# Kernel optimization log

Measured on AMD Instinct MI355X. Metric: run time of the kernel, lower is better.

The kernel has to match this reference:

```python
import jax, jax.numpy as jnp
import numpy as np

B, T, C, H = 2048, 128, 256, 64

def setup_inputs() -> dict:
    key = jax.random.key(0)
    kx, kk, kq, kv = jax.random.split(key, 4)
    s = 1.0 / np.sqrt(C)  # nn.Linear default init scale (approx)
    return {
        "x": jax.random.normal(kx, (B, T, C), dtype=jnp.float32),
        "Wk": jax.random.uniform(kk, (C, H), jnp.float32, -s, s),
        "Wq": jax.random.uniform(kq, (C, H), jnp.float32, -s, s),
        "Wv": jax.random.uniform(kv, (C, H), jnp.float32, -s, s),
    }

def reference(x, Wk, Wq, Wv):
    # x: [B,T,C]; projections to [B,T,H]
    k = jnp.einsum('btc,ch->bth', x, Wk)
    q = jnp.einsum('btc,ch->bth', x, Wq)
    v = jnp.einsum('btc,ch->bth', x, Wv)
    # NOTE: original scales by C**-0.5 (input dim), not head_size**-0.5
    scale = jnp.asarray(C, x.dtype) ** -0.5
    wei = jnp.einsum('bth,bsh->bts', q, k) * scale  # [B,T,T]
    causal = jnp.tril(jnp.ones((T, T), dtype=bool))
    wei = jnp.where(causal, wei, -jnp.inf)
    wei = jax.nn.softmax(wei, axis=-1)
    # dropout is identity in eval mode (deterministic reference)
    return jnp.einsum('bts,bsh->bth', wei, v)
```

## Files before the change

kernel.cpp:

```cpp
#include <hip/hip_runtime.h>

typedef __bf16 bf16;
typedef __bf16 bf16x4 __attribute__((ext_vector_type(4)));
typedef __bf16 bf16x8 __attribute__((ext_vector_type(8)));
typedef float  f32x4  __attribute__((ext_vector_type(4)));

#define B_ 2048
#define T_ 128
#define C_ 256
#define H_ 64

#define SMEM_BYTES 54272

__global__ void wt_kernel(const float* __restrict__ Wk, const float* __restrict__ Wq,
                          const float* __restrict__ Wv, bf16* __restrict__ Wt) {
    int o = blockIdx.x * 256 + threadIdx.x;
    int slot = o >> 14;
    int h    = (o & 16383) >> 8;
    int cc   = o & 255;
    const float* src = (slot == 0) ? Wq : (slot == 1 ? Wk : Wv);
    Wt[o] = (bf16)src[cc * 64 + h];
}

__global__ void __launch_bounds__(256, 3)
attn_kernel(const float* __restrict__ xg, const bf16* __restrict__ Wt,
            float* __restrict__ outg) {
    __shared__ __align__(16) char smem_raw[SMEM_BYTES];
    bf16* xs  = (bf16*)smem_raw;
    bf16* Wsm = (bf16*)(smem_raw + 18432);
    bf16* Qs  = (bf16*)smem_raw;
    bf16* Ks  = (bf16*)(smem_raw + 18432);
    bf16* Vt  = (bf16*)(smem_raw + 36864);
    bf16* Ps  = (bf16*)smem_raw;

    const int tid  = threadIdx.x;
    const int b    = blockIdx.x;
    const int w    = tid >> 6;
    const int lane = tid & 63;
    const int quad = lane >> 4;
    const int n16  = lane & 15;

    const f32x4 zero4 = {0.f, 0.f, 0.f, 0.f};

    f32x4 acc[2][12];
    #pragma unroll
    for (int mt = 0; mt < 2; mt++)
        #pragma unroll
        for (int nt = 0; nt < 12; nt++) acc[mt][nt] = zero4;

    const float*  xb  = xg + (size_t)b * (T_ * C_);
    const ushort* WtU = (const ushort*)Wt;

    for (int c = 0; c < 4; c++) {
        __syncthreads();
        #pragma unroll
        for (int i = 0; i < 8; i++) {
            int f  = tid + 256 * i;
            int t  = f >> 4;
            int c4 = (f & 15) * 4;
            float4 v = *(const float4*)(xb + t * C_ + c * 64 + c4);
            bf16x4 bv = {(bf16)v.x, (bf16)v.y, (bf16)v.z, (bf16)v.w};
            *(bf16x4*)(xs + t * 72 + c4) = bv;
        }
        #pragma unroll
        for (int i = 0; i < 12; i++) {
            int g    = tid + 256 * i;
            int slot = g >> 10;
            int rem  = g & 1023;
            int h    = rem >> 4;
            int c4   = (rem & 15) * 4;
            ushort4 wv = *(const ushort4*)(WtU + slot * 16384 + h * 256 + c * 64 + c4);
            *(ushort4*)((ushort*)Wsm + (slot * 64 + h) * 72 + c4) = wv;
        }
        __syncthreads();
        bf16x8 a[2][2];
        #pragma unroll
        for (int mt = 0; mt < 2; mt++)
            #pragma unroll
            for (int ks = 0; ks < 2; ks++)
                a[mt][ks] = *(const bf16x8*)(xs + (16 * (2 * w + mt) + n16) * 72 + 32 * ks + 8 * quad);
        #pragma unroll
        for (int nt = 0; nt < 12; nt++) {
            int row = ((nt >> 2) * 64 + 16 * (nt & 3) + n16) * 72 + 8 * quad;
            bf16x8 b0 = *(const bf16x8*)(Wsm + row);
            bf16x8 b1 = *(const bf16x8*)(Wsm + row + 32);
            #pragma unroll
            for (int mt = 0; mt < 2; mt++) {
                acc[mt][nt] = __builtin_amdgcn_mfma_f32_16x16x32_bf16(a[mt][0], b0, acc[mt][nt], 0, 0, 0);
                acc[mt][nt] = __builtin_amdgcn_mfma_f32_16x16x32_bf16(a[mt][1], b1, acc[mt][nt], 0, 0, 0);
            }
        }
    }
    __syncthreads();

    #pragma unroll
    for (int mt = 0; mt < 2; mt++) {
        int tbase = 16 * (2 * w + mt) + 4 * quad;
        #pragma unroll
        for (int nt = 0; nt < 8; nt++) {
            bf16* dst = (nt < 4) ? Qs : Ks;
            int h = 16 * (nt & 3) + n16;
            #pragma unroll
            for (int r = 0; r < 4; r++)
                dst[(tbase + r) * 72 + h] = (bf16)acc[mt][nt][r];
        }
        #pragma unroll
        for (int nt = 8; nt < 12; nt++) {
            int h = 16 * (nt - 8) + n16;
            bf16x4 pv = {(bf16)acc[mt][nt][0], (bf16)acc[mt][nt][1],
                         (bf16)acc[mt][nt][2], (bf16)acc[mt][nt][3]};
            *(bf16x4*)(Vt + h * 136 + tbase) = pv;
        }
    }
    __syncthreads();

    f32x4 sacc[2][8];
    int mts[2] = {w, 7 - w};
    #pragma unroll
    for (int half = 0; half < 2; half++) {
        int mt = mts[half];
        int sT = ((mt >> 1) + 1) * 2;
        bf16x8 qa[2];
        #pragma unroll
        for (int ks = 0; ks < 2; ks++)
            qa[ks] = *(const bf16x8*)(Qs + (16 * mt + n16) * 72 + 32 * ks + 8 * quad);
        #pragma unroll
        for (int nt = 0; nt < 8; nt++) {
            sacc[half][nt] = zero4;
            if (nt < sT) {
                bf16x8 kb0 = *(const bf16x8*)(Ks + (16 * nt + n16) * 72 + 8 * quad);
                bf16x8 kb1 = *(const bf16x8*)(Ks + (16 * nt + n16) * 72 + 32 + 8 * quad);
                sacc[half][nt] = __builtin_amdgcn_mfma_f32_16x16x32_bf16(qa[0], kb0, sacc[half][nt], 0, 0, 0);
                sacc[half][nt] = __builtin_amdgcn_mfma_f32_16x16x32_bf16(qa[1], kb1, sacc[half][nt], 0, 0, 0);
            }
        }
        #pragma unroll
        for (int r = 0; r < 4; r++) {
            int t = 16 * mt + 4 * quad + r;
            float mx = -3.0e38f;
            #pragma unroll
            for (int nt = 0; nt < 8; nt++) {
                if (nt < sT) {
                    float v = sacc[half][nt][r] * 0.0625f;
                    v = (16 * nt + n16 <= t) ? v : -3.0e38f;
                    sacc[half][nt][r] = v;
                    mx = fmaxf(mx, v);
                }
            }
            mx = fmaxf(mx, __shfl_xor(mx, 1));
            mx = fmaxf(mx, __shfl_xor(mx, 2));
            mx = fmaxf(mx, __shfl_xor(mx, 4));
            mx = fmaxf(mx, __shfl_xor(mx, 8));
            float sum = 0.f;
            #pragma unroll
            for (int nt = 0; nt < 8; nt++) {
                if (nt < sT) {
                    float p = __builtin_amdgcn_exp2f((sacc[half][nt][r] - mx) * 1.4426950408889634f);
                    sacc[half][nt][r] = p;
                    sum += p;
                }
            }
            sum += __shfl_xor(sum, 1);
            sum += __shfl_xor(sum, 2);
            sum += __shfl_xor(sum, 4);
            sum += __shfl_xor(sum, 8);
            float rinv = 1.0f / sum;
            #pragma unroll
            for (int nt = 0; nt < 8; nt++)
                if (nt < sT) sacc[half][nt][r] *= rinv;
        }
    }
    __syncthreads();

    #pragma unroll
    for (int half = 0; half < 2; half++) {
        int mt = mts[half];
        int sT = ((mt >> 1) + 1) * 2;
        #pragma unroll
        for (int nt = 0; nt < 8; nt++) {
            if (nt < sT) {
                #pragma unroll
                for (int r = 0; r < 4; r++)
                    Ps[(16 * mt + 4 * quad + r) * 136 + 16 * nt + n16] = (bf16)sacc[half][nt][r];
            }
        }
    }
    __syncthreads();

    #pragma unroll
    for (int half = 0; half < 2; half++) {
        int mt  = mts[half];
        int kst = (mt >> 1) + 1;
        f32x4 oacc[4];
        #pragma unroll
        for (int nt = 0; nt < 4; nt++) oacc[nt] = zero4;
        #pragma unroll
        for (int ks = 0; ks < 4; ks++) {
            if (ks < kst) {
                bf16x8 pa = *(const bf16x8*)(Ps + (16 * mt + n16) * 136 + 32 * ks + 8 * quad);
                #pragma unroll
                for (int nt = 0; nt < 4; nt++) {
                    bf16x8 vb = *(const bf16x8*)(Vt + (16 * nt + n16) * 136 + 32 * ks + 8 * quad);
                    oacc[nt] = __builtin_amdgcn_mfma_f32_16x16x32_bf16(pa, vb, oacc[nt], 0, 0, 0);
                }
            }
        }
        float* ob = outg + ((size_t)b * T_ + 16 * mt + 4 * quad) * H_;
        #pragma unroll
        for (int nt = 0; nt < 4; nt++)
            #pragma unroll
            for (int r = 0; r < 4; r++)
                ob[r * H_ + 16 * nt + n16] = oacc[nt][r];
    }
}

extern "C" void kernel_launch(void* const* d_in, const int* in_sizes, int n_in,
                              void* d_out, int out_size, void* d_ws, size_t ws_size,
                              hipStream_t stream) {
    const float* x  = (const float*)d_in[0];
    const float* Wk = (const float*)d_in[1];
    const float* Wq = (const float*)d_in[2];
    const float* Wv = (const float*)d_in[3];
    bf16* Wt = (bf16*)d_ws;
    wt_kernel<<<192, 256, 0, stream>>>(Wk, Wq, Wv, Wt);
    attn_kernel<<<B_, 256, 0, stream>>>(x, Wt, (float*)d_out);
}
```

Measured before the change: 494.5 us.

## Double-buffer x chunks via registers, read weights from global, stage output stores

The projection loop now prefetches the next x chunk into registers while computing on the current one, with two shared-memory x buffers so each chunk needs one barrier instead of two. Weight fragments are read straight from global (L2-resident, coalesced after the weight-transpose kernel now writes its output in scattered order) instead of being staged through shared memory. The final output is written through a padded shared buffer so the global stores become coalesced float4 writes. In exchange it adds register pressure and per-block global weight traffic, plus extra barriers at the end.

After: 541.6 us. 1.1x slower.

```diff
diff --git a/kernel.cpp b/kernel.cpp
--- a/kernel.cpp
+++ b/kernel.cpp
@@ -16,22 +16,24 @@
                           const float* __restrict__ Wv, bf16* __restrict__ Wt) {
     int o = blockIdx.x * 256 + threadIdx.x;
     int slot = o >> 14;
-    int h    = (o & 16383) >> 8;
-    int cc   = o & 255;
+    int r    = o & 16383;
+    int cc   = r >> 6;
+    int h    = r & 63;
     const float* src = (slot == 0) ? Wq : (slot == 1 ? Wk : Wv);
-    Wt[o] = (bf16)src[cc * 64 + h];
+    Wt[slot * 16384 + h * 256 + cc] = (bf16)src[r];
 }
 
 __global__ void __launch_bounds__(256, 3)
 attn_kernel(const float* __restrict__ xg, const bf16* __restrict__ Wt,
             float* __restrict__ outg) {
     __shared__ __align__(16) char smem_raw[SMEM_BYTES];
-    bf16* xs  = (bf16*)smem_raw;
-    bf16* Wsm = (bf16*)(smem_raw + 18432);
+    bf16* xb0 = (bf16*)smem_raw;
+    bf16* xb1 = (bf16*)(smem_raw + 18432);
     bf16* Qs  = (bf16*)smem_raw;
     bf16* Ks  = (bf16*)(smem_raw + 18432);
     bf16* Vt  = (bf16*)(smem_raw + 36864);
     bf16* Ps  = (bf16*)smem_raw;
+    float* Of = (float*)smem_raw;
 
     const int tid  = threadIdx.x;
     const int b    = blockIdx.x;
@@ -51,28 +53,32 @@
     const float*  xb  = xg + (size_t)b * (T_ * C_);
     const ushort* WtU = (const ushort*)Wt;
 
+    float4 xr[8];
+    #pragma unroll
+    for (int i = 0; i < 8; i++) {
+        int f = tid + 256 * i;
+        int t = f >> 4, c4 = (f & 15) * 4;
+        xr[i] = *(const float4*)(xb + t * C_ + c4);
+    }
+    #pragma unroll
+    for (int i = 0; i < 8; i++) {
+        int f = tid + 256 * i;
+        int t = f >> 4, c4 = (f & 15) * 4;
+        bf16x4 bv = {(bf16)xr[i].x, (bf16)xr[i].y, (bf16)xr[i].z, (bf16)xr[i].w};
+        *(bf16x4*)(xb0 + t * 72 + c4) = bv;
+    }
+
     for (int c = 0; c < 4; c++) {
+        if (c < 3) {
+            #pragma unroll
+            for (int i = 0; i < 8; i++) {
+                int f = tid + 256 * i;
+                int t = f >> 4, c4 = (f & 15) * 4;
+                xr[i] = *(const float4*)(xb + t * C_ + (c + 1) * 64 + c4);
+            }
+        }
         __syncthreads();
-        #pragma unroll
-        for (int i = 0; i < 8; i++) {
-            int f  = tid + 256 * i;
-            int t  = f >> 4;
-            int c4 = (f & 15) * 4;
-            float4 v = *(const float4*)(xb + t * C_ + c * 64 + c4);
-            bf16x4 bv = {(bf16)v.x, (bf16)v.y, (bf16)v.z, (bf16)v.w};
-            *(bf16x4*)(xs + t * 72 + c4) = bv;
-        }
-        #pragma unroll
-        for (int i = 0; i < 12; i++) {
-            int g    = tid + 256 * i;
-            int slot = g >> 10;
-            int rem  = g & 1023;
-            int h    = rem >> 4;
-            int c4   = (rem & 15) * 4;
-            ushort4 wv = *(const ushort4*)(WtU + slot * 16384 + h * 256 + c * 64 + c4);
-            *(ushort4*)((ushort*)Wsm + (slot * 64 + h) * 72 + c4) = wv;
-        }
-        __syncthreads();
+        const bf16* xs = (c & 1) ? xb1 : xb0;
         bf16x8 a[2][2];
         #pragma unroll
         for (int mt = 0; mt < 2; mt++)
@@ -81,13 +87,23 @@
                 a[mt][ks] = *(const bf16x8*)(xs + (16 * (2 * w + mt) + n16) * 72 + 32 * ks + 8 * quad);
         #pragma unroll
         for (int nt = 0; nt < 12; nt++) {
-            int row = ((nt >> 2) * 64 + 16 * (nt & 3) + n16) * 72 + 8 * quad;
-            bf16x8 b0 = *(const bf16x8*)(Wsm + row);
-            bf16x8 b1 = *(const bf16x8*)(Wsm + row + 32);
+            const ushort* wp = WtU + (nt >> 2) * 16384 + (16 * (nt & 3) + n16) * 256 + c * 64 + 8 * quad;
+            bf16x8 b0 = *(const bf16x8*)(wp);
+            bf16x8 b1 = *(const bf16x8*)(wp + 32);
             #pragma unroll
             for (int mt = 0; mt < 2; mt++) {
                 acc[mt][nt] = __builtin_amdgcn_mfma_f32_16x16x32_bf16(a[mt][0], b0, acc[mt][nt], 0, 0, 0);
                 acc[mt][nt] = __builtin_amdgcn_mfma_f32_16x16x32_bf16(a[mt][1], b1, acc[mt][nt], 0, 0, 0);
+            }
+        }
+        if (c < 3) {
+            bf16* dstb = (c & 1) ? xb0 : xb1;
+            #pragma unroll
+            for (int i = 0; i < 8; i++) {
+                int f = tid + 256 * i;
+                int t = f >> 4, c4 = (f & 15) * 4;
+                bf16x4 bv = {(bf16)xr[i].x, (bf16)xr[i].y, (bf16)xr[i].z, (bf16)xr[i].w};
+                *(bf16x4*)(dstb + t * 72 + c4) = bv;
             }
         }
     }
@@ -187,13 +203,13 @@
     }
     __syncthreads();
 
+    f32x4 oacc[2][4];
     #pragma unroll
     for (int half = 0; half < 2; half++) {
         int mt  = mts[half];
         int kst = (mt >> 1) + 1;
-        f32x4 oacc[4];
-        #pragma unroll
-        for (int nt = 0; nt < 4; nt++) oacc[nt] = zero4;
+        #pragma unroll
+        for (int nt = 0; nt < 4; nt++) oacc[half][nt] = zero4;
         #pragma unroll
         for (int ks = 0; ks < 4; ks++) {
             if (ks < kst) {
@@ -201,16 +217,29 @@
                 #pragma unroll
                 for (int nt = 0; nt < 4; nt++) {
                     bf16x8 vb = *(const bf16x8*)(Vt + (16 * nt + n16) * 136 + 32 * ks + 8 * quad);
-                    oacc[nt] = __builtin_amdgcn_mfma_f32_16x16x32_bf16(pa, vb, oacc[nt], 0, 0, 0);
+                    oacc[half][nt] = __builtin_amdgcn_mfma_f32_16x16x32_bf16(pa, vb, oacc[half][nt], 0, 0, 0);
                 }
             }
         }
-        float* ob = outg + ((size_t)b * T_ + 16 * mt + 4 * quad) * H_;
+    }
+    __syncthreads();
+
+    #pragma unroll
+    for (int half = 0; half < 2; half++) {
+        int mt = mts[half];
         #pragma unroll
         for (int nt = 0; nt < 4; nt++)
             #pragma unroll
             for (int r = 0; r < 4; r++)
-                ob[r * H_ + 16 * nt + n16] = oacc[nt][r];
+                Of[(16 * mt + 4 * quad + r) * 68 + 16 * nt + n16] = oacc[half][nt][r];
+    }
+    __syncthreads();
+    #pragma unroll
+    for (int i = 0; i < 8; i++) {
+        int f = tid + 256 * i;
+        int t = f >> 4, h4 = (f & 15) * 4;
+        float4 v = *(const float4*)(Of + t * 68 + h4);
+        *(float4*)(outg + ((size_t)b * T_ + t) * H_ + h4) = v;
     }
 }
 
```
